# Optimization experiments

Measured on AMD Instinct MI355X. Metric: run time of the kernel, lower is better.

Reference implementation:

```python
import jax, jax.numpy as jnp
import numpy as np

N_NODES = 50000
N_EDGES = 800000
HEADS = 8
DIM = 32
NEG_SLOPE = 0.2


def setup_inputs() -> dict:
    key = jax.random.key(0)
    k1, k2, k3, k4, k5 = jax.random.split(key, 5)
    feat = jax.random.normal(k1, (N_NODES, HEADS * DIM), dtype=jnp.float32)
    attn_l = jax.random.normal(k2, (1, HEADS, DIM), dtype=jnp.float32)
    attn_r = jax.random.normal(k3, (1, HEADS, DIM), dtype=jnp.float32)
    src_idx = jax.random.randint(k4, (N_EDGES,), 0, N_NODES, dtype=jnp.int32)
    dst_idx = jnp.sort(jax.random.randint(k5, (N_EDGES,), 0, N_NODES, dtype=jnp.int32))
    return {"feat": feat, "attn_l": attn_l, "attn_r": attn_r,
            "src_idx": src_idx, "dst_idx": dst_idx}


def reference(feat, attn_l, attn_r, src_idx, dst_idx):
    # [N, H, D] node features
    h = feat.reshape(-1, HEADS, DIM)
    n = h.shape[0]
    # per-node attention logits: [N, H]
    el = jnp.sum(h * attn_l, axis=-1)
    er = jnp.sum(h * attn_r, axis=-1)
    # edge scores e = leaky_relu(el[u] + er[v]): [E, H]
    e = jax.nn.leaky_relu(el[src_idx] + er[dst_idx], negative_slope=NEG_SLOPE)
    # segment softmax over incoming edges of each dst node
    e_max = jax.ops.segment_max(e, dst_idx, num_segments=n)          # [N, H]
    e_exp = jnp.exp(e - e_max[dst_idx])                              # [E, H]
    denom = jax.ops.segment_sum(e_exp, dst_idx, num_segments=n)     # [N, H]
    a = e_exp / denom[dst_idx]                                      # [E, H]
    # weighted scatter-sum aggregation: sum_{u in N(v)} a_uv * h_u
    m = h[src_idx] * a[:, :, None]                                  # [E, H, D]
    out = jax.ops.segment_sum(m, dst_idx, num_segments=n)           # [N, H, D]
    return out
```

## Files before the change

kernel.cpp:

```cpp
#include <hip/hip_runtime.h>
#include <hip/hip_fp16.h>
#include <math.h>

#define HEADS 8
#define DIM 32
#define NEG_SLOPE 0.2f

typedef float f32x4 __attribute__((ext_vector_type(4)));

__device__ inline float2 u2f2(unsigned int u) {
    __half2 h = __builtin_bit_cast(__half2, u);
    return __half22float2(h);
}
__device__ inline unsigned short f2bf(float f) {
    unsigned int u = __builtin_bit_cast(unsigned int, f);
    u += 0x7FFFu + ((u >> 16) & 1u);
    return (unsigned short)(u >> 16);
}
__device__ inline float bf2f(unsigned short b) {
    unsigned int u = ((unsigned int)b) << 16;
    return __builtin_bit_cast(float, u);
}

__global__ __launch_bounds__(256) void gat_prep_kernel(
    const float4* __restrict__ feat4,
    const float4* __restrict__ attn_l4,
    const float4* __restrict__ attn_r4,
    float* __restrict__ el_n,
    float* __restrict__ er_n,
    uint2* __restrict__ feat_h2,
    const int* __restrict__ dst,
    int* __restrict__ rowptr,
    int n_nodes, int n_edges, int nb_logits) {
    int b = blockIdx.x;
    if (b < nb_logits) {
        int wid = (b * 256 + threadIdx.x) >> 6;
        if (wid >= n_nodes) return;
        int lane = threadIdx.x & 63;
        int h = lane >> 3;
        int q = lane & 7;

        float4 al = attn_l4[lane];
        float4 ar = attn_r4[lane];
        float4 v  = feat4[(size_t)wid * 64 + lane];

        float sl = v.x * al.x + v.y * al.y + v.z * al.z + v.w * al.w;
        float sr = v.x * ar.x + v.y * ar.y + v.z * ar.z + v.w * ar.w;
#pragma unroll
        for (int off = 1; off < 8; off <<= 1) {
            sl += __shfl_xor(sl, off, 64);
            sr += __shfl_xor(sr, off, 64);
        }
        if (q == 0) {
            el_n[(unsigned)wid * 8 + h] = sl;
            er_n[(unsigned)wid * 8 + h] = sr;
        }
        uint2 o;
        o.x = __builtin_bit_cast(unsigned int, __floats2half2_rn(v.x, v.y));
        o.y = __builtin_bit_cast(unsigned int, __floats2half2_rn(v.z, v.w));
        feat_h2[(size_t)wid * 64 + lane] = o;
    } else {
        int e = (b - nb_logits) * 256 + threadIdx.x;
        if (e >= n_edges) return;
        int d = dst[e];
        int prev = (e > 0) ? dst[e - 1] : -1;
        for (int v = prev + 1; v <= d; ++v) rowptr[v] = e;
        if (e == n_edges - 1) {
            for (int v = d + 1; v <= n_nodes; ++v) rowptr[v] = n_edges;
        }
    }
}

__global__ __launch_bounds__(256) void gat_wprep_kernel(
    const float* __restrict__ el_n,
    const float* __restrict__ er_n,
    const int* __restrict__ src_idx,
    const int* __restrict__ rowptr,
    unsigned short* __restrict__ w_e,
    float* __restrict__ inv_den,
    int n_nodes) {
    int vraw = (blockIdx.x * blockDim.x + threadIdx.x) >> 6;
    if (vraw >= n_nodes) return;
    int v = __builtin_amdgcn_readfirstlane(vraw);
    int lane = threadIdx.x & 63;
    int s = lane >> 3;
    int h = lane & 7;

    int start = __builtin_amdgcn_readfirstlane(rowptr[v]);
    int end   = __builtin_amdgcn_readfirstlane(rowptr[v + 1]);
    if (start == end) return;

    float er_vh = er_n[(unsigned)v * 8 + h];

    float den = 0.f;
    for (int e0 = start; e0 < end; e0 += 8) {
        int e = e0 + s;
        int ee = e < end ? e : (end - 1);
        int u = src_idx[ee];
        float sc = el_n[(unsigned)u * 8 + h] + er_vh;
        sc = fmaxf(sc, NEG_SLOPE * sc);
        float w = __expf(sc);
        unsigned short wb = f2bf(w);
        float wf = bf2f(wb);
        if (e < end) {
            w_e[(size_t)e * 8 + h] = wb;
            den += wf;
        }
    }
    den += __shfl_xor(den, 8, 64);
    den += __shfl_xor(den, 16, 64);
    den += __shfl_xor(den, 32, 64);
    if (s == 0) {
        inv_den[(unsigned)v * 8 + h] = 1.f / den;
    }
}

__global__ __launch_bounds__(256) void gat_aggregate_kernel(
    const uint2* __restrict__ feat_h,
    const unsigned short* __restrict__ w_e,
    const float* __restrict__ inv_den,
    const int* __restrict__ src_idx,
    const int* __restrict__ rowptr,
    f32x4* __restrict__ out4,
    int n_nodes) {
    int vraw = (blockIdx.x * blockDim.x + threadIdx.x) >> 6;
    if (vraw >= n_nodes) return;
    int v = __builtin_amdgcn_readfirstlane(vraw);
    int lane = threadIdx.x & 63;
    int h = lane >> 3;

    int start = __builtin_amdgcn_readfirstlane(rowptr[v]);
    int end   = __builtin_amdgcn_readfirstlane(rowptr[v + 1]);

    unsigned obase = ((unsigned)v << 6) + (unsigned)lane;
    if (start == end) {
        f32x4 z = {0.f, 0.f, 0.f, 0.f};
        __builtin_nontemporal_store(z, &out4[obase]);
        return;
    }
    int endm1 = end - 1;

    f32x4 acc0 = {0.f, 0.f, 0.f, 0.f};
    f32x4 acc1 = {0.f, 0.f, 0.f, 0.f};

    for (int e = start; e < end; e += 8) {
        int   idx[8];
        uint2 fr[8];
        float wv[8];
#pragma unroll
        for (int i = 0; i < 8; ++i) {
            int ee = (e + i < endm1) ? (e + i) : endm1;
            idx[i] = src_idx[ee];
            wv[i]  = bf2f(w_e[(size_t)ee * 8 + h]);
            if (e + i > endm1) wv[i] = 0.f;
        }
#pragma unroll
        for (int i = 0; i < 8; ++i) {
            fr[i] = feat_h[((unsigned)idx[i] << 6) + (unsigned)lane];
        }
#pragma unroll
        for (int i = 0; i < 8; ++i) {
            float w = wv[i];
            float2 lo = u2f2(fr[i].x);
            float2 hi = u2f2(fr[i].y);
            if (i & 1) {
                acc1.x += w * lo.x; acc1.y += w * lo.y;
                acc1.z += w * hi.x; acc1.w += w * hi.y;
            } else {
                acc0.x += w * lo.x; acc0.y += w * lo.y;
                acc0.z += w * hi.x; acc0.w += w * hi.y;
            }
        }
    }
    float invd = inv_den[((unsigned)v << 3) + (unsigned)h];
    f32x4 r = acc0 + acc1;
    r.x *= invd; r.y *= invd; r.z *= invd; r.w *= invd;
    __builtin_nontemporal_store(r, &out4[obase]);
}

extern "C" void kernel_launch(void* const* d_in, const int* in_sizes, int n_in,
                              void* d_out, int out_size, void* d_ws, size_t ws_size,
                              hipStream_t stream) {
    const float* feat   = (const float*)d_in[0];
    const float* attn_l = (const float*)d_in[1];
    const float* attn_r = (const float*)d_in[2];
    const int*   src    = (const int*)d_in[3];
    const int*   dst    = (const int*)d_in[4];
    float* out = (float*)d_out;

    int n_edges = in_sizes[3];
    int n_nodes = out_size / (HEADS * DIM);
    int nh = n_nodes * HEADS;

    char* ws = (char*)d_ws;
    float* el_n = (float*)ws;                     ws += (size_t)nh * 4;
    float* er_n = (float*)ws;                     ws += (size_t)nh * 4;
    float* inv_den = (float*)ws;                  ws += (size_t)nh * 4;
    int* rowptr = (int*)ws;                       ws += (size_t)(n_nodes + 1) * 4;
    ws = (char*)(((uintptr_t)ws + 15) & ~(uintptr_t)15);
    uint2* feat_h2 = (uint2*)ws;                  ws += (size_t)nh * 64;
    unsigned short* w_e = (unsigned short*)ws;

    int nb_logits = (n_nodes + 3) / 4;
    int nb_rowptr = (n_edges + 255) / 256;
    hipLaunchKernelGGL(gat_prep_kernel,
                       dim3(nb_logits + nb_rowptr), dim3(256), 0, stream,
                       (const float4*)feat, (const float4*)attn_l,
                       (const float4*)attn_r, el_n, er_n, feat_h2,
                       dst, rowptr, n_nodes, n_edges, nb_logits);

    hipLaunchKernelGGL(gat_wprep_kernel,
                       dim3((n_nodes + 3) / 4), dim3(256), 0, stream,
                       el_n, er_n, src, rowptr, w_e, inv_den, n_nodes);

    hipLaunchKernelGGL(gat_aggregate_kernel,
                       dim3((n_nodes + 3) / 4), dim3(256), 0, stream,
                       feat_h2, w_e, inv_den, src, rowptr, (f32x4*)out,
                       n_nodes);
}
```

Baseline: 110.2 us.

## Compute edge weights per edge thread and fold softmax denominator into aggregation

```diff
diff --git a/kernel.cpp b/kernel.cpp
--- a/kernel.cpp
+++ b/kernel.cpp
@@ -29,96 +29,76 @@
     float* __restrict__ el_n,
     float* __restrict__ er_n,
     uint2* __restrict__ feat_h2,
-    const int* __restrict__ dst,
-    int* __restrict__ rowptr,
-    int n_nodes, int n_edges, int nb_logits) {
-    int b = blockIdx.x;
-    if (b < nb_logits) {
-        int wid = (b * 256 + threadIdx.x) >> 6;
-        if (wid >= n_nodes) return;
-        int lane = threadIdx.x & 63;
-        int h = lane >> 3;
-        int q = lane & 7;
+    int n_nodes) {
+    int wid = (blockIdx.x * blockDim.x + threadIdx.x) >> 6;
+    if (wid >= n_nodes) return;
+    int lane = threadIdx.x & 63;
+    int h = lane >> 3;
+    int q = lane & 7;
 
-        float4 al = attn_l4[lane];
-        float4 ar = attn_r4[lane];
-        float4 v  = feat4[(size_t)wid * 64 + lane];
+    float4 al = attn_l4[lane];
+    float4 ar = attn_r4[lane];
+    float4 v  = feat4[(size_t)wid * 64 + lane];
 
-        float sl = v.x * al.x + v.y * al.y + v.z * al.z + v.w * al.w;
-        float sr = v.x * ar.x + v.y * ar.y + v.z * ar.z + v.w * ar.w;
+    float sl = v.x * al.x + v.y * al.y + v.z * al.z + v.w * al.w;
+    float sr = v.x * ar.x + v.y * ar.y + v.z * ar.z + v.w * ar.w;
 #pragma unroll
-        for (int off = 1; off < 8; off <<= 1) {
-            sl += __shfl_xor(sl, off, 64);
-            sr += __shfl_xor(sr, off, 64);
-        }
-        if (q == 0) {
-            el_n[(unsigned)wid * 8 + h] = sl;
-            er_n[(unsigned)wid * 8 + h] = sr;
-        }
-        uint2 o;
-        o.x = __builtin_bit_cast(unsigned int, __floats2half2_rn(v.x, v.y));
-        o.y = __builtin_bit_cast(unsigned int, __floats2half2_rn(v.z, v.w));
-        feat_h2[(size_t)wid * 64 + lane] = o;
-    } else {
-        int e = (b - nb_logits) * 256 + threadIdx.x;
-        if (e >= n_edges) return;
-        int d = dst[e];
-        int prev = (e > 0) ? dst[e - 1] : -1;
-        for (int v = prev + 1; v <= d; ++v) rowptr[v] = e;
-        if (e == n_edges - 1) {
-            for (int v = d + 1; v <= n_nodes; ++v) rowptr[v] = n_edges;
-        }
+    for (int off = 1; off < 8; off <<= 1) {
+        sl += __shfl_xor(sl, off, 64);
+        sr += __shfl_xor(sr, off, 64);
     }
+    if (q == 0) {
+        el_n[(unsigned)wid * 8 + h] = sl;
+        er_n[(unsigned)wid * 8 + h] = sr;
+    }
+    uint2 o;
+    o.x = __builtin_bit_cast(unsigned int, __floats2half2_rn(v.x, v.y));
+    o.y = __builtin_bit_cast(unsigned int, __floats2half2_rn(v.z, v.w));
+    feat_h2[(size_t)wid * 64 + lane] = o;
 }
 
-__global__ __launch_bounds__(256) void gat_wprep_kernel(
-    const float* __restrict__ el_n,
-    const float* __restrict__ er_n,
+__global__ __launch_bounds__(256) void gat_edgew_kernel(
+    const float4* __restrict__ el_n4,
+    const float4* __restrict__ er_n4,
     const int* __restrict__ src_idx,
-    const int* __restrict__ rowptr,
-    unsigned short* __restrict__ w_e,
-    float* __restrict__ inv_den,
-    int n_nodes) {
-    int vraw = (blockIdx.x * blockDim.x + threadIdx.x) >> 6;
-    if (vraw >= n_nodes) return;
-    int v = __builtin_amdgcn_readfirstlane(vraw);
-    int lane = threadIdx.x & 63;
-    int s = lane >> 3;
-    int h = lane & 7;
+    const int* __restrict__ dst_idx,
+    int* __restrict__ rowptr,
+    uint4* __restrict__ w_e4,
+    int n_edges, int n_nodes) {
+    int e = blockIdx.x * blockDim.x + threadIdx.x;
+    if (e >= n_edges) return;
+    int d = dst_idx[e];
+    int prev = (e > 0) ? dst_idx[e - 1] : -1;
+    for (int v = prev + 1; v <= d; ++v) rowptr[v] = e;
+    if (e == n_edges - 1) {
+        for (int v = d + 1; v <= n_nodes; ++v) rowptr[v] = n_edges;
+    }
 
-    int start = __builtin_amdgcn_readfirstlane(rowptr[v]);
-    int end   = __builtin_amdgcn_readfirstlane(rowptr[v + 1]);
-    if (start == end) return;
-
-    float er_vh = er_n[(unsigned)v * 8 + h];
-
-    float den = 0.f;
-    for (int e0 = start; e0 < end; e0 += 8) {
-        int e = e0 + s;
-        int ee = e < end ? e : (end - 1);
-        int u = src_idx[ee];
-        float sc = el_n[(unsigned)u * 8 + h] + er_vh;
-        sc = fmaxf(sc, NEG_SLOPE * sc);
-        float w = __expf(sc);
-        unsigned short wb = f2bf(w);
-        float wf = bf2f(wb);
-        if (e < end) {
-            w_e[(size_t)e * 8 + h] = wb;
-            den += wf;
-        }
+    unsigned u = (unsigned)src_idx[e];
+    float4 elA = el_n4[u * 2], elB = el_n4[u * 2 + 1];
+    float4 erA = er_n4[(unsigned)d * 2], erB = er_n4[(unsigned)d * 2 + 1];
+    float s[8];
+    s[0] = elA.x + erA.x; s[1] = elA.y + erA.y;
+    s[2] = elA.z + erA.z; s[3] = elA.w + erA.w;
+    s[4] = elB.x + erB.x; s[5] = elB.y + erB.y;
+    s[6] = elB.z + erB.z; s[7] = elB.w + erB.w;
+    unsigned short wb[8];
+#pragma unroll
+    for (int h = 0; h < 8; ++h) {
+        float t = fmaxf(s[h], NEG_SLOPE * s[h]);
+        wb[h] = f2bf(__expf(t));
     }
-    den += __shfl_xor(den, 8, 64);
-    den += __shfl_xor(den, 16, 64);
-    den += __shfl_xor(den, 32, 64);
-    if (s == 0) {
-        inv_den[(unsigned)v * 8 + h] = 1.f / den;
-    }
+    uint4 pk;
+    pk.x = (unsigned)wb[0] | ((unsigned)wb[1] << 16);
+    pk.y = (unsigned)wb[2] | ((unsigned)wb[3] << 16);
+    pk.z = (unsigned)wb[4] | ((unsigned)wb[5] << 16);
+    pk.w = (unsigned)wb[6] | ((unsigned)wb[7] << 16);
+    w_e4[e] = pk;
 }
 
 __global__ __launch_bounds__(256) void gat_aggregate_kernel(
     const uint2* __restrict__ feat_h,
     const unsigned short* __restrict__ w_e,
-    const float* __restrict__ inv_den,
     const int* __restrict__ src_idx,
     const int* __restrict__ rowptr,
     f32x4* __restrict__ out4,
@@ -140,6 +120,7 @@
     }
     int endm1 = end - 1;
 
+    float denA = 0.f, denB = 0.f;
     f32x4 acc0 = {0.f, 0.f, 0.f, 0.f};
     f32x4 acc1 = {0.f, 0.f, 0.f, 0.f};
 
@@ -164,15 +145,17 @@
             float2 lo = u2f2(fr[i].x);
             float2 hi = u2f2(fr[i].y);
             if (i & 1) {
+                denB += w;
                 acc1.x += w * lo.x; acc1.y += w * lo.y;
                 acc1.z += w * hi.x; acc1.w += w * hi.y;
             } else {
+                denA += w;
                 acc0.x += w * lo.x; acc0.y += w * lo.y;
                 acc0.z += w * hi.x; acc0.w += w * hi.y;
             }
         }
     }
-    float invd = inv_den[((unsigned)v << 3) + (unsigned)h];
+    float invd = 1.f / (denA + denB);
     f32x4 r = acc0 + acc1;
     r.x *= invd; r.y *= invd; r.z *= invd; r.w *= invd;
     __builtin_nontemporal_store(r, &out4[obase]);
@@ -195,26 +178,22 @@
     char* ws = (char*)d_ws;
     float* el_n = (float*)ws;                     ws += (size_t)nh * 4;
     float* er_n = (float*)ws;                     ws += (size_t)nh * 4;
-    float* inv_den = (float*)ws;                  ws += (size_t)nh * 4;
     int* rowptr = (int*)ws;                       ws += (size_t)(n_nodes + 1) * 4;
     ws = (char*)(((uintptr_t)ws + 15) & ~(uintptr_t)15);
     uint2* feat_h2 = (uint2*)ws;                  ws += (size_t)nh * 64;
     unsigned short* w_e = (unsigned short*)ws;
 
-    int nb_logits = (n_nodes + 3) / 4;
-    int nb_rowptr = (n_edges + 255) / 256;
     hipLaunchKernelGGL(gat_prep_kernel,
-                       dim3(nb_logits + nb_rowptr), dim3(256), 0, stream,
+                       dim3((n_nodes + 3) / 4), dim3(256), 0, stream,
                        (const float4*)feat, (const float4*)attn_l,
-                       (const float4*)attn_r, el_n, er_n, feat_h2,
-                       dst, rowptr, n_nodes, n_edges, nb_logits);
+                       (const float4*)attn_r, el_n, er_n, feat_h2, n_nodes);
 
-    hipLaunchKernelGGL(gat_wprep_kernel,
-                       dim3((n_nodes + 3) / 4), dim3(256), 0, stream,
-                       el_n, er_n, src, rowptr, w_e, inv_den, n_nodes);
+    hipLaunchKernelGGL(gat_edgew_kernel,
+                       dim3((n_edges + 255) / 256), dim3(256), 0, stream,
+                       (const float4*)el_n, (const float4*)er_n, src, dst,
+                       rowptr, (uint4*)w_e, n_edges, n_nodes);
 
     hipLaunchKernelGGL(gat_aggregate_kernel,
                        dim3((n_nodes + 3) / 4), dim3(256), 0, stream,
-                       feat_h2, w_e, inv_den, src, rowptr, (f32x4*)out,
-                       n_nodes);
+                       feat_h2, w_e, src, rowptr, (f32x4*)out, n_nodes);
 }
```

Result: faster. 96.07 us (-12.8%).
